# Performance work log

Measured on AMD Instinct MI355X. Metric: run time of the kernel, lower is better.

The kernel has to match this reference:

```python
import jax, jax.numpy as jnp
import numpy as np

N_RAYS = 16384
NUM_SAMPLES = 96
B = 1
D = H = W = 128          # input grid spatial size (grid layout [B, D, H, W, C])
OD = OH = OW = 128       # output grid spatial size
C_IN = 32                # input_grid_chn == ray encoding dim
C_HID = 32               # mlp_hidden_chn
C_OUT = 16               # grid_chn

CORNERS = [(dz, dy, dx) for dz in (0, 1) for dy in (0, 1) for dx in (0, 1)]


def _tri_setup(pts, sx, sy, sz):
    # pts [M,3] in normalized [-1,1]; axis 0 -> x (W), 1 -> y (H), 2 -> z (D).
    # align_corners=False convention (matches torch grid_sample default).
    cx = ((pts[:, 0] + 1.0) * sx - 1.0) * 0.5
    cy = ((pts[:, 1] + 1.0) * sy - 1.0) * 0.5
    cz = ((pts[:, 2] + 1.0) * sz - 1.0) * 0.5
    x0 = jnp.floor(cx); y0 = jnp.floor(cy); z0 = jnp.floor(cz)
    fx = cx - x0; fy = cy - y0; fz = cz - z0
    return x0.astype(jnp.int32), y0.astype(jnp.int32), z0.astype(jnp.int32), fx, fy, fz


def _corner_idx_w(x0, y0, z0, fx, fy, fz, bidx, dz, dy, dx, sx, sy, sz):
    # flat voxel index into a [B, sz, sy, sx] grid + trilinear weight (border clamp)
    ix = jnp.clip(x0 + dx, 0, sx - 1)
    iy = jnp.clip(y0 + dy, 0, sy - 1)
    iz = jnp.clip(z0 + dz, 0, sz - 1)
    w = ((fx if dx else 1.0 - fx) * (fy if dy else 1.0 - fy) * (fz if dz else 1.0 - fz))
    flat = ((bidx * sz + iz) * sy + iy) * sx + ix
    return flat, w


def _forward(origins, directions, near, far, encoding, grid_idx, input_grid, W0, b0, W1, b1):
    # 1) sample NUM_SAMPLES points per ray between near and far
    tvals = jnp.linspace(0.0, 1.0, NUM_SAMPLES)
    t = near[:, None] + (far - near)[:, None] * tvals[None, :]                 # [N,S]
    pts = (origins[:, None, :] + t[:, :, None] * directions[:, None, :]).reshape(-1, 3)  # [M,3]
    bidx = jnp.broadcast_to(grid_idx[:, None], (N_RAYS, NUM_SAMPLES)).reshape(-1)

    # 2) trilinear gather of point features from input_grid
    x0, y0, z0, fx, fy, fz = _tri_setup(pts, W, H, D)
    gflat = input_grid.reshape(B * D * H * W, C_IN)
    feat = jnp.zeros((pts.shape[0], C_IN), input_grid.dtype)
    for dz, dy, dx in CORNERS:  # fixed 8-corner loop, no [M,8,C] intermediate
        fi, w = _corner_idx_w(x0, y0, z0, fx, fy, fz, bidx, dz, dy, dx, W, H, D)
        feat = feat + w[:, None] * gflat[fi]

    # 3) add ray encoding, run the small MLP (relu hidden, linear output)
    enc = jnp.broadcast_to(encoding[:, None, :], (N_RAYS, NUM_SAMPLES, C_IN)).reshape(-1, C_IN)
    x = feat + enc
    h = jax.nn.relu(x @ W0 + b0)
    o = h @ W1 + b1                                                            # [M,C_OUT]

    # 4) trilinear scatter-splat of MLP output into the output grid
    xo, yo, zo, fxo, fyo, fzo = _tri_setup(pts, OW, OH, OD)
    out = jnp.zeros((B * OD * OH * OW, C_OUT), o.dtype)
    for dz, dy, dx in CORNERS:
        fo, w = _corner_idx_w(xo, yo, zo, fxo, fyo, fzo, bidx, dz, dy, dx, OW, OH, OD)
        out = out.at[fo].add(w[:, None] * o)
    return out.reshape(B, OD, OH, OW, C_OUT)


def setup_inputs() -> dict:
    key = jax.random.key(0)
    ks = jax.random.split(key, 8)
    origins = jax.random.uniform(ks[0], (N_RAYS, 3), minval=-0.5, maxval=0.5)
    d = jax.random.normal(ks[1], (N_RAYS, 3))
    directions = d / jnp.linalg.norm(d, axis=1, keepdims=True)
    near = 0.05 + 0.1 * jax.random.uniform(ks[2], (N_RAYS,))
    far = 1.0 + 0.5 * jax.random.uniform(ks[3], (N_RAYS,))
    encoding = 0.1 * jax.random.normal(ks[4], (N_RAYS, C_IN))
    grid_idx = jnp.zeros((N_RAYS,), dtype=jnp.int32)
    input_grid = 0.1 * jax.random.normal(ks[5], (B, D, H, W, C_IN))
    W0 = jax.random.normal(ks[6], (C_IN, C_HID)) / np.sqrt(C_IN)
    b0 = jnp.zeros((C_HID,), jnp.float32)
    W1 = jax.random.normal(ks[7], (C_HID, C_OUT)) / np.sqrt(C_HID)
    b1 = jnp.zeros((C_OUT,), jnp.float32)
    return {"origins": origins, "directions": directions, "near": near, "far": far,
            "encoding": encoding, "grid_idx": grid_idx, "input_grid": input_grid,
            "W0": W0, "b0": b0, "W1": W1, "b1": b1}


def reference(origins, directions, near, far, encoding, grid_idx, input_grid, W0, b0, W1, b1):
    return _forward(origins, directions, near, far, encoding, grid_idx, input_grid, W0, b0, W1, b1)
```

## Files before the change

kernel.cpp:

```cpp
#include <hip/hip_runtime.h>

#define N_RAYS 16384
#define NSAMP  96
#define GD 128
#define GH 128
#define GW 128
#define C_IN  32
#define C_HID 32
#define C_OUT 16
#define M_PTS (N_RAYS * NSAMP)
#define TPA 16
#define NTILES (TPA*TPA*TPA)
#define TW 8
#define TVOX (TW*TW*TW)
#define CHUNK 128

__device__ __forceinline__ int clampi(int v, int hi) { return min(max(v, 0), hi); }

struct TileSpan { int txa, txb, tya, tyb, tza, tzb; };
__device__ __forceinline__ TileSpan tile_span(int X, int Y, int Z) {
    TileSpan s;
    s.txa = clampi(X,   GW-1) >> 3;  s.txb = clampi(X+1, GW-1) >> 3;
    s.tya = clampi(Y,   GH-1) >> 3;  s.tyb = clampi(Y+1, GH-1) >> 3;
    s.tza = clampi(Z,   GD-1) >> 3;  s.tzb = clampi(Z+1, GD-1) >> 3;
    return s;
}

__global__ __launch_bounds__(256) void k1_point(
    const float* __restrict__ origins, const float* __restrict__ dirs,
    const float* __restrict__ nearv,   const float* __restrict__ farv,
    const float* __restrict__ enc,     const int*   __restrict__ gidx,
    const float* __restrict__ grid,    const float* __restrict__ W0,
    const float* __restrict__ b0,      const float* __restrict__ W1,
    const float* __restrict__ b1,
    float4* __restrict__ pf, float4* __restrict__ po, unsigned* __restrict__ counts)
{
    __shared__ __attribute__((aligned(16))) char smem[49152];
    uint2*    sOffW = (uint2*)smem;
    float4*   sFeat = (float4*)(smem + 16384);
    unsigned* lcnt  = (unsigned*)smem;

    int tid = threadIdx.x;
    int pid = blockIdx.x * 256 + tid;
    int ray = pid / NSAMP;
    int s   = pid - ray * NSAMP;

    float nr = nearv[ray], fr = farv[ray];
    float t  = nr + (fr - nr) * ((float)s * (1.0f / (NSAMP - 1)));
    float px = fmaf(t, dirs[ray*3+0], origins[ray*3+0]);
    float py = fmaf(t, dirs[ray*3+1], origins[ray*3+1]);
    float pz = fmaf(t, dirs[ray*3+2], origins[ray*3+2]);
    int   b  = gidx[ray];

    float cx = ((px + 1.0f) * (float)GW - 1.0f) * 0.5f;
    float cy = ((py + 1.0f) * (float)GH - 1.0f) * 0.5f;
    float cz = ((pz + 1.0f) * (float)GD - 1.0f) * 0.5f;
    float fxf = floorf(cx), fyf = floorf(cy), fzf = floorf(cz);
    float fx = cx - fxf, fy = cy - fyf, fz = cz - fzf;
    int X = (int)fxf, Y = (int)fyf, Z = (int)fzf;

    int gx[2] = { clampi(X, GW-1), clampi(X+1, GW-1) };
    int gy[2] = { clampi(Y, GH-1), clampi(Y+1, GH-1) };
    int gz[2] = { clampi(Z, GD-1), clampi(Z+1, GD-1) };
    float wxa[2] = { 1.0f - fx, fx };
    float wya[2] = { 1.0f - fy, fy };
    float wza[2] = { 1.0f - fz, fz };

    #pragma unroll
    for (int dz = 0; dz < 2; ++dz)
    #pragma unroll
    for (int dy = 0; dy < 2; ++dy)
    #pragma unroll
    for (int dx = 0; dx < 2; ++dx) {
        const int ci = dz*4 + dy*2 + dx;
        unsigned flat = ((((unsigned)b * GD + gz[dz]) * GH + gy[dy]) * GW + gx[dx]) * C_IN;
        float w = wza[dz] * wya[dy] * wxa[dx];
        sOffW[tid*8 + ci] = make_uint2(flat, __float_as_uint(w));
    }
    __syncthreads();

    int lane  = tid & 63;
    int wbase = tid & ~63;
    int sub   = lane >> 3;
    int q     = lane & 7;
    #pragma unroll
    for (int g = 0; g < 8; ++g) {
        int p = wbase + g*8 + sub;
        float4 acc = make_float4(0.0f, 0.0f, 0.0f, 0.0f);
        #pragma unroll
        for (int c = 0; c < 8; ++c) {
            uint2 ow = sOffW[p*8 + c];
            const float4* src = (const float4*)(grid + ow.x);
            float4 v = src[q];
            float wgt = __uint_as_float(ow.y);
            acc.x = fmaf(wgt, v.x, acc.x);
            acc.y = fmaf(wgt, v.y, acc.y);
            acc.z = fmaf(wgt, v.z, acc.z);
            acc.w = fmaf(wgt, v.w, acc.w);
        }
        sFeat[p*8 + ((q + p) & 7)] = acc;
    }
    __syncthreads();

    float feat[C_IN];
    {
        const float4* e4 = (const float4*)(enc + (size_t)ray * C_IN);
        #pragma unroll
        for (int qq = 0; qq < 8; ++qq) {
            float4 fv = sFeat[tid*8 + ((qq + tid) & 7)];
            float4 ev = e4[qq];
            feat[4*qq+0] = fv.x + ev.x;
            feat[4*qq+1] = fv.y + ev.y;
            feat[4*qq+2] = fv.z + ev.z;
            feat[4*qq+3] = fv.w + ev.w;
        }
    }
    for (int i = tid; i < NTILES; i += 256) lcnt[i] = 0;

    float h[C_HID];
    #pragma unroll
    for (int j = 0; j < C_HID; ++j) h[j] = b0[j];
    #pragma unroll
    for (int i = 0; i < C_IN; ++i) {
        float xi = feat[i];
        #pragma unroll
        for (int j = 0; j < C_HID; ++j) h[j] = fmaf(xi, W0[i*C_HID + j], h[j]);
    }
    #pragma unroll
    for (int j = 0; j < C_HID; ++j) h[j] = fmaxf(h[j], 0.0f);

    float o[C_OUT];
    #pragma unroll
    for (int j = 0; j < C_OUT; ++j) o[j] = b1[j];
    #pragma unroll
    for (int i = 0; i < C_HID; ++i) {
        float hi = h[i];
        #pragma unroll
        for (int j = 0; j < C_OUT; ++j) o[j] = fmaf(hi, W1[i*C_OUT + j], o[j]);
    }

    unsigned key = ((unsigned)(X + 256) & 511u)
                 | (((unsigned)(Y + 256) & 511u) << 9)
                 | (((unsigned)(Z + 256) & 511u) << 18);
    pf[pid] = make_float4(fx, fy, fz, __uint_as_float(key));
    #pragma unroll
    for (int qq = 0; qq < 4; ++qq)
        po[(size_t)qq * M_PTS + pid] = make_float4(o[4*qq+0], o[4*qq+1], o[4*qq+2], o[4*qq+3]);

    __syncthreads();
    TileSpan ts = tile_span(X, Y, Z);
    #pragma unroll
    for (int ez = 0; ez < 2; ++ez) {
        if (ez && ts.tzb == ts.tza) continue;
        #pragma unroll
        for (int ey = 0; ey < 2; ++ey) {
            if (ey && ts.tyb == ts.tya) continue;
            #pragma unroll
            for (int ex = 0; ex < 2; ++ex) {
                if (ex && ts.txb == ts.txa) continue;
                int tt = ((ts.tza + ez) * TPA + (ts.tya + ey)) * TPA + (ts.txa + ex);
                atomicAdd(&lcnt[tt], 1u);
            }
        }
    }
    __syncthreads();
    for (int i = tid; i < NTILES; i += 256)
        if (lcnt[i]) atomicAdd(&counts[i], lcnt[i]);
}

__global__ __launch_bounds__(256) void k2_scan(
    const unsigned* __restrict__ counts,
    unsigned* __restrict__ offsets, unsigned* __restrict__ alloc,
    unsigned* __restrict__ order)
{
    __shared__ unsigned psum[256];
    __shared__ unsigned bh[256];
    __shared__ unsigned bb[256];
    int tid = threadIdx.x;
    unsigned base = tid * 16;
    unsigned ssum = 0;
    for (int i = 0; i < 16; ++i) ssum += counts[base + i];
    psum[tid] = ssum;
    bh[tid] = 0;
    __syncthreads();
    if (tid == 0) {
        unsigned r = 0;
        for (int i = 0; i < 256; ++i) { unsigned v = psum[i]; psum[i] = r; r += v; }
    }
    __syncthreads();
    unsigned run = psum[tid];
    for (int i = 0; i < 16; ++i) {
        unsigned v = counts[base + i];
        offsets[base + i] = run;
        alloc[base + i]   = run;
        run += v;
        atomicAdd(&bh[min(v >> 4, 255u)], 1u);
    }
    __syncthreads();
    if (tid == 0) {
        unsigned r = 0;
        for (int b = 255; b >= 0; --b) { unsigned v = bh[b]; bb[b] = r; r += v; }
    }
    __syncthreads();
    for (int i = 0; i < 16; ++i) {
        unsigned v = counts[base + i];
        unsigned slot = atomicAdd(&bb[min(v >> 4, 255u)], 1u);
        order[slot] = base + i;
    }
}

__global__ __launch_bounds__(256) void k3_scatter(
    const float4* __restrict__ pf, unsigned* __restrict__ alloc,
    unsigned* __restrict__ entries)
{
    __shared__ unsigned lcnt[NTILES];
    __shared__ unsigned lbase[NTILES];
    for (int i = threadIdx.x; i < NTILES; i += 256) lcnt[i] = 0;
    __syncthreads();

    int pid = blockIdx.x * 256 + threadIdx.x;
    float4 f = pf[pid];
    unsigned key = __float_as_uint(f.w);
    int X = (int)(key & 511u) - 256;
    int Y = (int)((key >> 9) & 511u) - 256;
    int Z = (int)((key >> 18) & 511u) - 256;
    TileSpan ts = tile_span(X, Y, Z);

    unsigned rnk[2][2][2];
    #pragma unroll
    for (int ez = 0; ez < 2; ++ez) {
        bool okz = (ez == 0) || (ts.tzb > ts.tza);
        #pragma unroll
        for (int ey = 0; ey < 2; ++ey) {
            bool oky = (ey == 0) || (ts.tyb > ts.tya);
            #pragma unroll
            for (int ex = 0; ex < 2; ++ex) {
                bool okx = (ex == 0) || (ts.txb > ts.txa);
                if (okz && oky && okx) {
                    int tt = ((ts.tza + ez) * TPA + (ts.tya + ey)) * TPA + (ts.txa + ex);
                    rnk[ez][ey][ex] = atomicAdd(&lcnt[tt], 1u);
                }
            }
        }
    }
    __syncthreads();
    for (int i = threadIdx.x; i < NTILES; i += 256)
        if (lcnt[i]) lbase[i] = atomicAdd(&alloc[i], lcnt[i]);
    __syncthreads();
    #pragma unroll
    for (int ez = 0; ez < 2; ++ez) {
        bool okz = (ez == 0) || (ts.tzb > ts.tza);
        #pragma unroll
        for (int ey = 0; ey < 2; ++ey) {
            bool oky = (ey == 0) || (ts.tyb > ts.tya);
            #pragma unroll
            for (int ex = 0; ex < 2; ++ex) {
                bool okx = (ex == 0) || (ts.txb > ts.txa);
                if (okz && oky && okx) {
                    int tt = ((ts.tza + ez) * TPA + (ts.tya + ey)) * TPA + (ts.txa + ex);
                    entries[lbase[tt] + rnk[ez][ey][ex]] = (unsigned)pid;
                }
            }
        }
    }
}

__global__ __launch_bounds__(256) void k4_accum(
    const float4* __restrict__ pf, const float4* __restrict__ po,
    const unsigned* __restrict__ entries, const unsigned* __restrict__ offsets,
    const unsigned* __restrict__ alloc, const unsigned* __restrict__ order,
    float* __restrict__ out)
{
    __shared__ __attribute__((aligned(16))) float4 sA[CHUNK];
    __shared__ __attribute__((aligned(16))) int    sZ[CHUNK];
    __shared__ __attribute__((aligned(16))) float4 sO[4*CHUNK];

    int t  = order[blockIdx.x];
    int tx = t & (TPA-1), ty = (t >> 4) & (TPA-1), tz = t >> 8;
    int ox = tx * TW, oy = ty * TW, oz = tz * TW;

    int tid  = threadIdx.x;
    int lane = tid & 63;
    int w    = tid >> 6;
    int vxa  = ox + (lane & 7);
    int vya  = oy + (lane >> 3);
    int l0   = 2*w, l1 = 2*w + 1;

    float accA[C_OUT], accB[C_OUT];
    #pragma unroll
    for (int c = 0; c < C_OUT; ++c) { accA[c] = 0.0f; accB[c] = 0.0f; }

    unsigned e0 = offsets[t], e1 = alloc[t];
    for (unsigned base = e0; base < e1; base += CHUNK) {
        int n = min((unsigned)CHUNK, e1 - base);
        if (tid < CHUNK) {
            if (tid < n) {
                unsigned p = entries[base + tid];
                float4 f = pf[p];
                unsigned key = __float_as_uint(f.w);
                int X = (int)(key & 511u) - 256;
                int Y = (int)((key >> 9) & 511u) - 256;
                int Z = (int)((key >> 18) & 511u) - 256;
                int cx0 = clampi(X, GW-1),  cx1 = clampi(X+1, GW-1);
                int cy0 = clampi(Y, GH-1),  cy1 = clampi(Y+1, GH-1);
                int cz0 = clampi(Z, GD-1),  cz1 = clampi(Z+1, GD-1);
                unsigned pk = (unsigned)cx0 | ((unsigned)cx1 << 8)
                            | ((unsigned)cy0 << 16) | ((unsigned)cy1 << 24);
                int st0 = ((unsigned)(cz0 - oz) < 8u) ? (cz0 - oz) : 255;
                int st1 = ((unsigned)(cz1 - oz) < 8u) ? (cz1 - oz) : 255;
                sA[tid] = make_float4(f.x, f.y, f.z, __uint_as_float(pk));
                sZ[tid] = st0 | (st1 << 8);
                #pragma unroll
                for (int q = 0; q < 4; ++q)
                    sO[q*CHUNK + tid] = po[(size_t)q * M_PTS + p];
            } else {
                sZ[tid] = 255 | (255 << 8);
            }
        }
        __syncthreads();

        const int4* sZ4 = (const int4*)sZ;
        int n4 = (n + 3) & ~3;
        for (int jb = 0; jb < n4; jb += 4) {
            int4 z4 = sZ4[jb >> 2];
            #pragma unroll
            for (int k = 0; k < 4; ++k) {
                int zz  = (k==0) ? z4.x : (k==1) ? z4.y : (k==2) ? z4.z : z4.w;
                int st0 = zz & 255, st1 = (zz >> 8) & 255;
                bool hitA = (st0 == l0) | (st1 == l0);
                bool hitB = (st0 == l1) | (st1 == l1);
                if (!(hitA | hitB)) continue;
                int j = jb + k;
                float4 a = sA[j];
                unsigned pk = __float_as_uint(a.w);
                int cx0 = (int)(pk & 255u),         cx1 = (int)((pk >> 8) & 255u);
                int cy0 = (int)((pk >> 16) & 255u), cy1 = (int)(pk >> 24);

                float wx = ((vxa == cx0) ? 1.0f - a.x : 0.0f)
                         + ((vxa == cx1) ? a.x        : 0.0f);
                float wy = ((vya == cy0) ? 1.0f - a.y : 0.0f)
                         + ((vya == cy1) ? a.y        : 0.0f);
                float wxy = wx * wy;

                if (hitA) {
                    float wzA = ((st0 == l0) ? 1.0f - a.z : 0.0f)
                              + ((st1 == l0) ? a.z        : 0.0f);
                    float wA = wxy * wzA;
                    #pragma unroll
                    for (int q = 0; q < 4; ++q) {
                        float4 ov = sO[q*CHUNK + j];
                        accA[4*q+0] = fmaf(wA, ov.x, accA[4*q+0]);
                        accA[4*q+1] = fmaf(wA, ov.y, accA[4*q+1]);
                        accA[4*q+2] = fmaf(wA, ov.z, accA[4*q+2]);
                        accA[4*q+3] = fmaf(wA, ov.w, accA[4*q+3]);
                    }
                }
                if (hitB) {
                    float wzB = ((st0 == l1) ? 1.0f - a.z : 0.0f)
                              + ((st1 == l1) ? a.z        : 0.0f);
                    float wB = wxy * wzB;
                    #pragma unroll
                    for (int q = 0; q < 4; ++q) {
                        float4 ov = sO[q*CHUNK + j];
                        accB[4*q+0] = fmaf(wB, ov.x, accB[4*q+0]);
                        accB[4*q+1] = fmaf(wB, ov.y, accB[4*q+1]);
                        accB[4*q+2] = fmaf(wB, ov.z, accB[4*q+2]);
                        accB[4*q+3] = fmaf(wB, ov.w, accB[4*q+3]);
                    }
                }
            }
        }
        __syncthreads();
    }

    size_t baseA = ((((size_t)(oz + l0)) * GH + vya) * GW + vxa) * C_OUT;
    size_t baseB = ((((size_t)(oz + l1)) * GH + vya) * GW + vxa) * C_OUT;
    #pragma unroll
    for (int q = 0; q < 4; ++q) {
        *(float4*)(out + baseA + 4*q) = make_float4(accA[4*q+0], accA[4*q+1], accA[4*q+2], accA[4*q+3]);
        *(float4*)(out + baseB + 4*q) = make_float4(accB[4*q+0], accB[4*q+1], accB[4*q+2], accB[4*q+3]);
    }
}

#define SEGS   8
#define SEGLEN (NSAMP / SEGS)
#define NTHREADS (N_RAYS * SEGS)

__global__ __launch_bounds__(256, 2) void splat_seg_kernel(
    const float* __restrict__ origins, const float* __restrict__ dirs,
    const float* __restrict__ nearv,   const float* __restrict__ farv,
    const float* __restrict__ enc,     const int*   __restrict__ gidx,
    const float* __restrict__ grid,    const float* __restrict__ W0,
    const float* __restrict__ b0,      const float* __restrict__ W1,
    const float* __restrict__ b1,      float* __restrict__ out)
{
    int tid = blockIdx.x * blockDim.x + threadIdx.x;
    if (tid >= NTHREADS) return;
    int ray = tid / SEGS;
    int seg = tid - ray * SEGS;
    float nr = nearv[ray], fr = farv[ray];
    float ox = origins[3*ray+0], oy = origins[3*ray+1], oz = origins[3*ray+2];
    float rdx = dirs[3*ray+0],   rdy = dirs[3*ray+1],   rdz = dirs[3*ray+2];
    int   b  = gidx[ray];
    float accv[8][C_OUT];
    #pragma unroll
    for (int sl = 0; sl < 8; ++sl)
        #pragma unroll
        for (int c = 0; c < C_OUT; ++c) accv[sl][c] = 0.0f;
    int Xp = 0, Yp = 0, Zp = 0;
    #pragma unroll 1
    for (int k = 0; k < SEGLEN; ++k) {
        int s = seg * SEGLEN + k;
        float t  = nr + (fr - nr) * ((float)s * (1.0f / (NSAMP - 1)));
        float px = fmaf(t, rdx, ox);
        float py = fmaf(t, rdy, oy);
        float pz = fmaf(t, rdz, oz);
        float cx = ((px + 1.0f) * (float)GW - 1.0f) * 0.5f;
        float cy = ((py + 1.0f) * (float)GH - 1.0f) * 0.5f;
        float cz = ((pz + 1.0f) * (float)GD - 1.0f) * 0.5f;
        float fxf = floorf(cx), fyf = floorf(cy), fzf = floorf(cz);
        float fx = cx - fxf, fy = cy - fyf, fz = cz - fzf;
        int X = (int)fxf, Y = (int)fyf, Z = (int)fzf;
        if (k == 0) { Xp = X; Yp = Y; Zp = Z; }
        else if (X != Xp || Y != Yp || Z != Zp) {
            bool fXm[2], fYm[2], fZm[2];
            int  vx[2], vy[2], vz[2];
            #pragma unroll
            for (int p = 0; p < 2; ++p) {
                int xo = Xp + ((Xp ^ p) & 1), xn = X + ((X ^ p) & 1);
                fXm[p] = (xo != xn);  vx[p] = clampi(xo, GW-1);
                int yo = Yp + ((Yp ^ p) & 1), yn = Y + ((Y ^ p) & 1);
                fYm[p] = (yo != yn);  vy[p] = clampi(yo, GH-1);
                int zo = Zp + ((Zp ^ p) & 1), zn = Z + ((Z ^ p) & 1);
                fZm[p] = (zo != zn);  vz[p] = clampi(zo, GD-1);
            }
            #pragma unroll
            for (int pxi = 0; pxi < 2; ++pxi)
            #pragma unroll
            for (int pyi = 0; pyi < 2; ++pyi)
            #pragma unroll
            for (int pzi = 0; pzi < 2; ++pzi) {
                const int sl = pxi*4 + pyi*2 + pzi;
                if (fXm[pxi] | fYm[pyi] | fZm[pzi]) {
                    size_t flat = ((((size_t)b * GD + vz[pzi]) * GH + vy[pyi]) * GW + vx[pxi]) * C_OUT;
                    float* op = out + flat;
                    #pragma unroll
                    for (int c = 0; c < C_OUT; ++c) { atomicAdd(op + c, accv[sl][c]); accv[sl][c] = 0.0f; }
                }
            }
            Xp = X; Yp = Y; Zp = Z;
        }
        float feat[C_IN];
        {
            const float4* e4 = (const float4*)(enc + (size_t)ray * C_IN);
            #pragma unroll
            for (int q = 0; q < C_IN/4; ++q) {
                float4 v = e4[q];
                feat[4*q+0] = v.x; feat[4*q+1] = v.y; feat[4*q+2] = v.z; feat[4*q+3] = v.w;
            }
        }
        int gx[2] = { clampi(X, GW-1), clampi(X+1, GW-1) };
        int gy[2] = { clampi(Y, GH-1), clampi(Y+1, GH-1) };
        int gz[2] = { clampi(Z, GD-1), clampi(Z+1, GD-1) };
        float wxa[2] = { 1.0f - fx, fx };
        float wya[2] = { 1.0f - fy, fy };
        float wza[2] = { 1.0f - fz, fz };
        #pragma unroll
        for (int dz = 0; dz < 2; ++dz)
        #pragma unroll
        for (int dy = 0; dy < 2; ++dy)
        #pragma unroll
        for (int dx = 0; dx < 2; ++dx) {
            float w = wza[dz] * wya[dy] * wxa[dx];
            size_t flat = ((((size_t)b * GD + gz[dz]) * GH + gy[dy]) * GW + gx[dx]) * C_IN;
            const float4* g4 = (const float4*)(grid + flat);
            #pragma unroll
            for (int q = 0; q < C_IN/4; ++q) {
                float4 v = g4[q];
                feat[4*q+0] = fmaf(w, v.x, feat[4*q+0]);
                feat[4*q+1] = fmaf(w, v.y, feat[4*q+1]);
                feat[4*q+2] = fmaf(w, v.z, feat[4*q+2]);
                feat[4*q+3] = fmaf(w, v.w, feat[4*q+3]);
            }
        }
        float h[C_HID];
        #pragma unroll
        for (int j = 0; j < C_HID; ++j) h[j] = b0[j];
        #pragma unroll
        for (int i = 0; i < C_IN; ++i) {
            float xi = feat[i];
            #pragma unroll
            for (int j = 0; j < C_HID; ++j) h[j] = fmaf(xi, W0[i*C_HID + j], h[j]);
        }
        #pragma unroll
        for (int j = 0; j < C_HID; ++j) h[j] = fmaxf(h[j], 0.0f);
        float o[C_OUT];
        #pragma unroll
        for (int j = 0; j < C_OUT; ++j) o[j] = b1[j];
        #pragma unroll
        for (int i = 0; i < C_HID; ++i) {
            float hi = h[i];
            #pragma unroll
            for (int j = 0; j < C_OUT; ++j) o[j] = fmaf(hi, W1[i*C_OUT + j], o[j]);
        }
        float wxs[2], wys[2], wzs[2];
        #pragma unroll
        for (int p = 0; p < 2; ++p) {
            wxs[p] = ((X & 1) == p) ? (1.0f - fx) : fx;
            wys[p] = ((Y & 1) == p) ? (1.0f - fy) : fy;
            wzs[p] = ((Z & 1) == p) ? (1.0f - fz) : fz;
        }
        #pragma unroll
        for (int pxi = 0; pxi < 2; ++pxi)
        #pragma unroll
        for (int pyi = 0; pyi < 2; ++pyi)
        #pragma unroll
        for (int pzi = 0; pzi < 2; ++pzi) {
            const int sl = pxi*4 + pyi*2 + pzi;
            float w = wxs[pxi] * wys[pyi] * wzs[pzi];
            #pragma unroll
            for (int c = 0; c < C_OUT; ++c) accv[sl][c] = fmaf(w, o[c], accv[sl][c]);
        }
    }
    #pragma unroll
    for (int pxi = 0; pxi < 2; ++pxi)
    #pragma unroll
    for (int pyi = 0; pyi < 2; ++pyi)
    #pragma unroll
    for (int pzi = 0; pzi < 2; ++pzi) {
        const int sl = pxi*4 + pyi*2 + pzi;
        int vx = clampi(Xp + ((Xp ^ pxi) & 1), GW-1);
        int vy = clampi(Yp + ((Yp ^ pyi) & 1), GH-1);
        int vz = clampi(Zp + ((Zp ^ pzi) & 1), GD-1);
        size_t flat = ((((size_t)b * GD + vz) * GH + vy) * GW + vx) * C_OUT;
        float* op = out + flat;
        #pragma unroll
        for (int c = 0; c < C_OUT; ++c) atomicAdd(op + c, accv[sl][c]);
    }
}

extern "C" void kernel_launch(void* const* d_in, const int* in_sizes, int n_in,
                              void* d_out, int out_size, void* d_ws, size_t ws_size,
                              hipStream_t stream) {
    const float* origins = (const float*)d_in[0];
    const float* dirs    = (const float*)d_in[1];
    const float* nearv   = (const float*)d_in[2];
    const float* farv    = (const float*)d_in[3];
    const float* enc     = (const float*)d_in[4];
    const int*   gidx    = (const int*)  d_in[5];
    const float* grid    = (const float*)d_in[6];
    const float* W0      = (const float*)d_in[7];
    const float* b0      = (const float*)d_in[8];
    const float* W1      = (const float*)d_in[9];
    const float* b1      = (const float*)d_in[10];
    float* out = (float*)d_out;

    const size_t PF_B = (size_t)M_PTS * 16;
    const size_t PO_B = (size_t)M_PTS * 64;
    const size_t EN_B = (size_t)M_PTS * 8 * 4;
    const size_t CT_B = (size_t)NTILES * 4;
    const size_t NEED = PF_B + PO_B + EN_B + 4 * CT_B;

    if (ws_size < NEED) {
        hipMemsetAsync(out, 0, (size_t)out_size * sizeof(float), stream);
        splat_seg_kernel<<<NTHREADS/256, 256, 0, stream>>>(
            origins, dirs, nearv, farv, enc, gidx, grid, W0, b0, W1, b1, out);
        return;
    }

    char* w = (char*)d_ws;
    float4*   pf      = (float4*)   w;              w += PF_B;
    float4*   po      = (float4*)   w;              w += PO_B;
    unsigned* entries = (unsigned*) w;              w += EN_B;
    unsigned* counts  = (unsigned*) w;              w += CT_B;
    unsigned* offsets = (unsigned*) w;              w += CT_B;
    unsigned* alloc   = (unsigned*) w;              w += CT_B;
    unsigned* order   = (unsigned*) w;              w += CT_B;

    hipMemsetAsync(counts, 0, CT_B, stream);
    k1_point<<<M_PTS/256, 256, 0, stream>>>(origins, dirs, nearv, farv, enc, gidx,
                                            grid, W0, b0, W1, b1, pf, po, counts);
    k2_scan<<<1, 256, 0, stream>>>(counts, offsets, alloc, order);
    k3_scatter<<<M_PTS/256, 256, 0, stream>>>(pf, alloc, entries);
    k4_accum<<<NTILES, 256, 0, stream>>>(pf, po, entries, offsets, alloc, order, out);
}
```

Baseline: 512.0 us.

## Use ballot bitmasks to skip non-hitting points and parallelize tile scans

In the accumulation kernel, each wave now builds per-wave 64-bit ballot masks of the points whose z-slab touches its voxel layers. Each wave then iterates only over the set bits, instead of scanning every point and testing it. The chunk size is doubled to 256 so all threads load entries. The scan kernel replaces serial single-thread prefix sums with wave shuffle scans and caches the counts in registers. The trade-off is extra ballot work and more shared memory per block.

```diff
diff --git a/kernel.cpp b/kernel.cpp
--- a/kernel.cpp
+++ b/kernel.cpp
@@ -13,7 +13,7 @@
 #define NTILES (TPA*TPA*TPA)
 #define TW 8
 #define TVOX (TW*TW*TW)
-#define CHUNK 128
+#define CHUNK 256
 
 __device__ __forceinline__ int clampi(int v, int hi) { return min(max(v, 0), hi); }
 
@@ -173,37 +173,55 @@
     unsigned* __restrict__ offsets, unsigned* __restrict__ alloc,
     unsigned* __restrict__ order)
 {
-    __shared__ unsigned psum[256];
+    __shared__ unsigned wsum[4], wbase[4];
+    __shared__ unsigned bwsum[4], bwbase[4];
     __shared__ unsigned bh[256];
     __shared__ unsigned bb[256];
-    int tid = threadIdx.x;
+    int tid = threadIdx.x, lane = tid & 63, wv = tid >> 6;
     unsigned base = tid * 16;
+    unsigned loc[16];
     unsigned ssum = 0;
-    for (int i = 0; i < 16; ++i) ssum += counts[base + i];
-    psum[tid] = ssum;
+    #pragma unroll
+    for (int i = 0; i < 16; ++i) { loc[i] = counts[base + i]; ssum += loc[i]; }
     bh[tid] = 0;
-    __syncthreads();
-    if (tid == 0) {
-        unsigned r = 0;
-        for (int i = 0; i < 256; ++i) { unsigned v = psum[i]; psum[i] = r; r += v; }
-    }
-    __syncthreads();
-    unsigned run = psum[tid];
+
+    unsigned x = ssum;
+    #pragma unroll
+    for (int d = 1; d < 64; d <<= 1) {
+        unsigned v = __shfl_up(x, d);
+        if (lane >= d) x += v;
+    }
+    if (lane == 63) wsum[wv] = x;
+    __syncthreads();
+    if (tid == 0) { unsigned r = 0; for (int ww = 0; ww < 4; ++ww) { wbase[ww] = r; r += wsum[ww]; } }
+    __syncthreads();
+    unsigned run = wbase[wv] + x - ssum;
+    #pragma unroll
     for (int i = 0; i < 16; ++i) {
-        unsigned v = counts[base + i];
+        unsigned v = loc[i];
         offsets[base + i] = run;
         alloc[base + i]   = run;
         run += v;
         atomicAdd(&bh[min(v >> 4, 255u)], 1u);
     }
     __syncthreads();
-    if (tid == 0) {
-        unsigned r = 0;
-        for (int b = 255; b >= 0; --b) { unsigned v = bh[b]; bb[b] = r; r += v; }
-    }
-    __syncthreads();
+
+    unsigned hv = bh[255 - tid];
+    unsigned y = hv;
+    #pragma unroll
+    for (int d = 1; d < 64; d <<= 1) {
+        unsigned v = __shfl_up(y, d);
+        if (lane >= d) y += v;
+    }
+    if (lane == 63) bwsum[wv] = y;
+    __syncthreads();
+    if (tid == 0) { unsigned r = 0; for (int ww = 0; ww < 4; ++ww) { bwbase[ww] = r; r += bwsum[ww]; } }
+    __syncthreads();
+    bb[255 - tid] = bwbase[wv] + y - hv;
+    __syncthreads();
+    #pragma unroll
     for (int i = 0; i < 16; ++i) {
-        unsigned v = counts[base + i];
+        unsigned v = loc[i];
         unsigned slot = atomicAdd(&bb[min(v >> 4, 255u)], 1u);
         order[slot] = base + i;
     }
@@ -274,6 +292,7 @@
     __shared__ __attribute__((aligned(16))) float4 sA[CHUNK];
     __shared__ __attribute__((aligned(16))) int    sZ[CHUNK];
     __shared__ __attribute__((aligned(16))) float4 sO[4*CHUNK];
+    __shared__ unsigned long long sMask[4][4];
 
     int t  = order[blockIdx.x];
     int tx = t & (TPA-1), ty = (t >> 4) & (TPA-1), tz = t >> 8;
@@ -293,45 +312,44 @@
     unsigned e0 = offsets[t], e1 = alloc[t];
     for (unsigned base = e0; base < e1; base += CHUNK) {
         int n = min((unsigned)CHUNK, e1 - base);
-        if (tid < CHUNK) {
-            if (tid < n) {
-                unsigned p = entries[base + tid];
-                float4 f = pf[p];
-                unsigned key = __float_as_uint(f.w);
-                int X = (int)(key & 511u) - 256;
-                int Y = (int)((key >> 9) & 511u) - 256;
-                int Z = (int)((key >> 18) & 511u) - 256;
-                int cx0 = clampi(X, GW-1),  cx1 = clampi(X+1, GW-1);
-                int cy0 = clampi(Y, GH-1),  cy1 = clampi(Y+1, GH-1);
-                int cz0 = clampi(Z, GD-1),  cz1 = clampi(Z+1, GD-1);
-                unsigned pk = (unsigned)cx0 | ((unsigned)cx1 << 8)
-                            | ((unsigned)cy0 << 16) | ((unsigned)cy1 << 24);
-                int st0 = ((unsigned)(cz0 - oz) < 8u) ? (cz0 - oz) : 255;
-                int st1 = ((unsigned)(cz1 - oz) < 8u) ? (cz1 - oz) : 255;
-                sA[tid] = make_float4(f.x, f.y, f.z, __uint_as_float(pk));
-                sZ[tid] = st0 | (st1 << 8);
-                #pragma unroll
-                for (int q = 0; q < 4; ++q)
-                    sO[q*CHUNK + tid] = po[(size_t)q * M_PTS + p];
-            } else {
-                sZ[tid] = 255 | (255 << 8);
-            }
+        int st0 = 255, st1 = 255;
+        if (tid < n) {
+            unsigned p = entries[base + tid];
+            float4 f = pf[p];
+            unsigned key = __float_as_uint(f.w);
+            int X = (int)(key & 511u) - 256;
+            int Y = (int)((key >> 9) & 511u) - 256;
+            int Z = (int)((key >> 18) & 511u) - 256;
+            int cx0 = clampi(X, GW-1),  cx1 = clampi(X+1, GW-1);
+            int cy0 = clampi(Y, GH-1),  cy1 = clampi(Y+1, GH-1);
+            int cz0 = clampi(Z, GD-1),  cz1 = clampi(Z+1, GD-1);
+            unsigned pk = (unsigned)cx0 | ((unsigned)cx1 << 8)
+                        | ((unsigned)cy0 << 16) | ((unsigned)cy1 << 24);
+            st0 = ((unsigned)(cz0 - oz) < 8u) ? (cz0 - oz) : 255;
+            st1 = ((unsigned)(cz1 - oz) < 8u) ? (cz1 - oz) : 255;
+            sA[tid] = make_float4(f.x, f.y, f.z, __uint_as_float(pk));
+            sZ[tid] = st0 | (st1 << 8);
+            #pragma unroll
+            for (int q = 0; q < 4; ++q)
+                sO[q*CHUNK + tid] = po[(size_t)q * M_PTS + p];
+        }
+        int w0 = st0 >> 1, w1 = st1 >> 1;
+        #pragma unroll
+        for (int tw = 0; tw < 4; ++tw) {
+            unsigned long long m = __ballot((w0 == tw) | (w1 == tw));
+            if (lane == 0) sMask[tw][tid >> 6] = m;
         }
         __syncthreads();
 
-        const int4* sZ4 = (const int4*)sZ;
-        int n4 = (n + 3) & ~3;
-        for (int jb = 0; jb < n4; jb += 4) {
-            int4 z4 = sZ4[jb >> 2];
-            #pragma unroll
-            for (int k = 0; k < 4; ++k) {
-                int zz  = (k==0) ? z4.x : (k==1) ? z4.y : (k==2) ? z4.z : z4.w;
-                int st0 = zz & 255, st1 = (zz >> 8) & 255;
-                bool hitA = (st0 == l0) | (st1 == l0);
-                bool hitB = (st0 == l1) | (st1 == l1);
-                if (!(hitA | hitB)) continue;
-                int j = jb + k;
+        #pragma unroll
+        for (int g = 0; g < 4; ++g) {
+            unsigned long long m = sMask[w][g];
+            while (m) {
+                int j = (g << 6) + (int)__builtin_ctzll(m);
+                m &= m - 1;
                 float4 a = sA[j];
+                int zz = sZ[j];
+                int s0 = zz & 255, s1 = (zz >> 8) & 255;
                 unsigned pk = __float_as_uint(a.w);
                 int cx0 = (int)(pk & 255u),         cx1 = (int)((pk >> 8) & 255u);
                 int cy0 = (int)((pk >> 16) & 255u), cy1 = (int)(pk >> 24);
@@ -342,9 +360,10 @@
                          + ((vya == cy1) ? a.y        : 0.0f);
                 float wxy = wx * wy;
 
+                bool hitA = (s0 == l0) | (s1 == l0);
                 if (hitA) {
-                    float wzA = ((st0 == l0) ? 1.0f - a.z : 0.0f)
-                              + ((st1 == l0) ? a.z        : 0.0f);
+                    float wzA = ((s0 == l0) ? 1.0f - a.z : 0.0f)
+                              + ((s1 == l0) ? a.z        : 0.0f);
                     float wA = wxy * wzA;
                     #pragma unroll
                     for (int q = 0; q < 4; ++q) {
@@ -355,9 +374,10 @@
                         accA[4*q+3] = fmaf(wA, ov.w, accA[4*q+3]);
                     }
                 }
+                bool hitB = (s0 == l1) | (s1 == l1);
                 if (hitB) {
-                    float wzB = ((st0 == l1) ? 1.0f - a.z : 0.0f)
-                              + ((st1 == l1) ? a.z        : 0.0f);
+                    float wzB = ((s0 == l1) ? 1.0f - a.z : 0.0f)
+                              + ((s1 == l1) ? a.z        : 0.0f);
                     float wB = wxy * wzB;
                     #pragma unroll
                     for (int q = 0; q < 4; ++q) {
```

After: 450.3 us. 12.0% less time.
